# Kernel tuning notes

Measured on AMD Instinct MI355X. Metric: run time of the kernel, lower is better.

## Reference

```python
import jax, jax.numpy as jnp
import numpy as np

WIN = (9, 9)
EPS = float(np.power(np.e, -15))  # e^-15 threshold from original code


def _box_sum(x, win):
    kernel = jnp.ones((1, 1, win[0], win[1]), dtype=x.dtype)
    p = win[0] // 2
    return jax.lax.conv_general_dilated(
        x, kernel, window_strides=(1, 1), padding=[(p, p), (p, p)],
        dimension_numbers=("NCHW", "OIHW", "NCHW"))


def setup_inputs() -> dict:
    key = jax.random.key(0)
    k1, k2 = jax.random.split(key)
    B, C, H, W = 32, 1, 512, 512
    I = jax.random.normal(k1, (B, C, H, W), dtype=jnp.float32)
    J = jax.random.normal(k2, (B, C, H, W), dtype=jnp.float32)
    return {"I": I, "J": J}


def reference(I, J):
    win = WIN
    win_size = win[0] * win[1]
    I_sum = _box_sum(I, win)
    J_sum = _box_sum(J, win)
    I2_sum = _box_sum(I * I, win)
    J2_sum = _box_sum(J * J, win)
    IJ_sum = _box_sum(I * J, win)

    u_I = I_sum / win_size
    u_J = J_sum / win_size
    cross = IJ_sum - u_J * I_sum - u_I * J_sum + u_I * u_J * win_size
    I_var = I2_sum - 2 * u_I * I_sum + u_I * u_I * win_size
    J_var = J2_sum - 2 * u_J * J_sum + u_J * u_J * win_size

    non_zero = I_var * J_var > EPS
    cross = jnp.where(non_zero, cross, 1.0)
    I_var = jnp.where(non_zero, I_var, 1.0)
    J_var = jnp.where(non_zero, J_var, 1.0)

    cc = cross * cross / (I_var * J_var + EPS)
    return -1.0 * jnp.mean(cc, axis=(1, 2, 3)) + 1.0
```

## Files before the change

kernel.cpp:

```cpp
#include <hip/hip_runtime.h>


#define IMG_H 512
#define IMG_W 512
#define NBATCH 32
#define RPW 8
#define STRIPS_PER_IMG (IMG_H / RPW)

__global__ __launch_bounds__(64, 2) void lcc_main(const float* __restrict__ I,
                                                  const float* __restrict__ J,
                                                  float* __restrict__ out) {
    const int lane  = threadIdx.x;
    const int strip = blockIdx.x;
    const int b  = strip / STRIPS_PER_IMG;
    const int y0 = (strip % STRIPS_PER_IMG) * RPW;
    const int x0 = lane * 8;

    const float* __restrict__ Ib = I + (size_t)b * IMG_H * IMG_W;
    const float* __restrict__ Jb = J + (size_t)b * IMG_H * IMG_W;

    auto load_row = [&](int y, float4& i0, float4& i1, float4& j0, float4& j1) {
        const float4* pI = reinterpret_cast<const float4*>(Ib + (size_t)y * IMG_W + x0);
        const float4* pJ = reinterpret_cast<const float4*>(Jb + (size_t)y * IMG_W + x0);
        i0 = pI[0]; i1 = pI[1]; j0 = pJ[0]; j1 = pJ[1];
    };

    float sI[8]  = {0.f,0.f,0.f,0.f,0.f,0.f,0.f,0.f};
    float sJ[8]  = {0.f,0.f,0.f,0.f,0.f,0.f,0.f,0.f};
    float sII[8] = {0.f,0.f,0.f,0.f,0.f,0.f,0.f,0.f};
    float sJJ[8] = {0.f,0.f,0.f,0.f,0.f,0.f,0.f,0.f};
    float sIJ[8] = {0.f,0.f,0.f,0.f,0.f,0.f,0.f,0.f};

    auto addv = [&](const float4& i0, const float4& i1,
                    const float4& j0, const float4& j1) {
        float iv[8] = {i0.x,i0.y,i0.z,i0.w,i1.x,i1.y,i1.z,i1.w};
        float jv[8] = {j0.x,j0.y,j0.z,j0.w,j1.x,j1.y,j1.z,j1.w};
        #pragma unroll
        for (int c = 0; c < 8; ++c) {
            sI[c]  += iv[c];
            sJ[c]  += jv[c];
            sII[c]  = fmaf(iv[c], iv[c], sII[c]);
            sJJ[c]  = fmaf(jv[c], jv[c], sJJ[c]);
            sIJ[c]  = fmaf(iv[c], jv[c], sIJ[c]);
        }
    };
    auto subv = [&](const float4& i0, const float4& i1,
                    const float4& j0, const float4& j1) {
        float iv[8] = {i0.x,i0.y,i0.z,i0.w,i1.x,i1.y,i1.z,i1.w};
        float jv[8] = {j0.x,j0.y,j0.z,j0.w,j1.x,j1.y,j1.z,j1.w};
        #pragma unroll
        for (int c = 0; c < 8; ++c) {
            sI[c]  -= iv[c];
            sJ[c]  -= jv[c];
            sII[c]  = fmaf(-iv[c], iv[c], sII[c]);
            sJJ[c]  = fmaf(-jv[c], jv[c], sJJ[c]);
            sIJ[c]  = fmaf(-iv[c], jv[c], sIJ[c]);
        }
    };

    auto hsum = [&](const float (&s)[8], float (&h)[8]) {
        float w[16];
        #pragma unroll
        for (int c = 0; c < 8; ++c) w[4+c] = s[c];
        #pragma unroll
        for (int c = 0; c < 4; ++c) {
            float a = __shfl_up(s[4+c], 1);
            w[c] = lane ? a : 0.f;
            a = __shfl_down(s[c], 1);
            w[12+c] = (lane < 63) ? a : 0.f;
        }
        float acc = 0.f;
        #pragma unroll
        for (int i = 0; i < 9; ++i) acc += w[i];
        h[0] = acc;
        #pragma unroll
        for (int k = 1; k < 8; ++k) { acc += w[k+8] - w[k-1]; h[k] = acc; }
    };

    #pragma unroll
    for (int k = 0; k < 9; ++k) {
        const int y = y0 - 4 + k;
        if (y >= 0) {
            float4 i0, i1, j0, j1;
            load_row(y, i0, i1, j0, j1);
            addv(i0, i1, j0, j1);
        }
    }

    const float inv81 = 1.0f / 81.0f;
    const float EPSV  = 3.0590232050182579e-07f;
    float local = 0.0f;

    #pragma unroll 1
    for (int r = 0; r < RPW; ++r) {
        const int t = y0 + r;

        const bool doadd = (r + 1 < RPW) && (t + 5 < IMG_H);
        const bool dosub = (r + 1 < RPW) && (t - 4 >= 0);
        float4 ai0 = {0,0,0,0}, ai1 = {0,0,0,0}, aj0 = {0,0,0,0}, aj1 = {0,0,0,0};
        float4 bi0 = {0,0,0,0}, bi1 = {0,0,0,0}, bj0 = {0,0,0,0}, bj1 = {0,0,0,0};
        if (doadd) load_row(t + 5, ai0, ai1, aj0, aj1);
        if (dosub) load_row(t - 4, bi0, bi1, bj0, bj1);

        float hI[8], hJ[8], hII[8], hJJ[8], hIJ[8];
        hsum(sI,  hI);
        hsum(sJ,  hJ);
        hsum(sII, hII);
        hsum(sJJ, hJJ);
        hsum(sIJ, hIJ);

        #pragma unroll
        for (int k = 0; k < 8; ++k) {
            float cross = fmaf(hI[k] * hJ[k], -inv81, hIJ[k]);
            float Iv    = fmaf(hI[k] * hI[k], -inv81, hII[k]);
            float Jv    = fmaf(hJ[k] * hJ[k], -inv81, hJJ[k]);
            float p  = Iv * Jv;
            bool  nz = p > EPSV;
            float c2 = nz ? cross : 1.0f;
            float p2 = nz ? p : 1.0f;
            local += (c2 * c2) * __builtin_amdgcn_rcpf(p2 + EPSV);
        }

        if (doadd) addv(ai0, ai1, aj0, aj1);
        if (dosub) subv(bi0, bi1, bj0, bj1);
    }

    #pragma unroll
    for (int off = 32; off > 0; off >>= 1) local += __shfl_down(local, off);
    if (lane == 0)
        atomicAdd(out + b, fmaf(local, -1.0f / (float)(IMG_H * IMG_W),
                                1.0f / (float)STRIPS_PER_IMG));
}

extern "C" void kernel_launch(void* const* d_in, const int* in_sizes, int n_in,
                              void* d_out, int out_size, void* d_ws, size_t ws_size,
                              hipStream_t stream) {
    const float* I = (const float*)d_in[0];
    const float* J = (const float*)d_in[1];
    float* out = (float*)d_out;

    const int total_strips = NBATCH * STRIPS_PER_IMG;
    lcc_main<<<total_strips, 64, 0, stream>>>(I, J, out);
}
```

Baseline: 118.2 us.

## Cache window rows in registers and prefetch next add row ahead

The 9 initial window rows are held in a register array, so the rows later subtracted from the running sums come from registers instead of being loaded from global memory again. The row to be added is prefetched one iteration ahead, and the row loop is fully unrolled so those loads overlap with the box-sum compute. This targets memory latency and redundant traffic in a kernel with little occupancy to hide latency. The cost is much higher VGPR use, which could limit occupancy or cause spills.

```diff
diff --git a/kernel.cpp b/kernel.cpp
--- a/kernel.cpp
+++ b/kernel.cpp
@@ -19,10 +19,10 @@
     const float* __restrict__ Ib = I + (size_t)b * IMG_H * IMG_W;
     const float* __restrict__ Jb = J + (size_t)b * IMG_H * IMG_W;
 
-    auto load_row = [&](int y, float4& i0, float4& i1, float4& j0, float4& j1) {
+    auto load_row = [&](int y, float4* d) {
         const float4* pI = reinterpret_cast<const float4*>(Ib + (size_t)y * IMG_W + x0);
         const float4* pJ = reinterpret_cast<const float4*>(Jb + (size_t)y * IMG_W + x0);
-        i0 = pI[0]; i1 = pI[1]; j0 = pJ[0]; j1 = pJ[1];
+        d[0] = pI[0]; d[1] = pI[1]; d[2] = pJ[0]; d[3] = pJ[1];
     };
 
     float sI[8]  = {0.f,0.f,0.f,0.f,0.f,0.f,0.f,0.f};
@@ -31,10 +31,9 @@
     float sJJ[8] = {0.f,0.f,0.f,0.f,0.f,0.f,0.f,0.f};
     float sIJ[8] = {0.f,0.f,0.f,0.f,0.f,0.f,0.f,0.f};
 
-    auto addv = [&](const float4& i0, const float4& i1,
-                    const float4& j0, const float4& j1) {
-        float iv[8] = {i0.x,i0.y,i0.z,i0.w,i1.x,i1.y,i1.z,i1.w};
-        float jv[8] = {j0.x,j0.y,j0.z,j0.w,j1.x,j1.y,j1.z,j1.w};
+    auto addv = [&](const float4* v) {
+        float iv[8] = {v[0].x,v[0].y,v[0].z,v[0].w,v[1].x,v[1].y,v[1].z,v[1].w};
+        float jv[8] = {v[2].x,v[2].y,v[2].z,v[2].w,v[3].x,v[3].y,v[3].z,v[3].w};
         #pragma unroll
         for (int c = 0; c < 8; ++c) {
             sI[c]  += iv[c];
@@ -44,10 +43,9 @@
             sIJ[c]  = fmaf(iv[c], jv[c], sIJ[c]);
         }
     };
-    auto subv = [&](const float4& i0, const float4& i1,
-                    const float4& j0, const float4& j1) {
-        float iv[8] = {i0.x,i0.y,i0.z,i0.w,i1.x,i1.y,i1.z,i1.w};
-        float jv[8] = {j0.x,j0.y,j0.z,j0.w,j1.x,j1.y,j1.z,j1.w};
+    auto subv = [&](const float4* v) {
+        float iv[8] = {v[0].x,v[0].y,v[0].z,v[0].w,v[1].x,v[1].y,v[1].z,v[1].w};
+        float jv[8] = {v[2].x,v[2].y,v[2].z,v[2].w,v[3].x,v[3].y,v[3].z,v[3].w};
         #pragma unroll
         for (int c = 0; c < 8; ++c) {
             sI[c]  -= iv[c];
@@ -77,30 +75,34 @@
         for (int k = 1; k < 8; ++k) { acc += w[k+8] - w[k-1]; h[k] = acc; }
     };
 
+    float4 W[9][4];
     #pragma unroll
     for (int k = 0; k < 9; ++k) {
-        const int y = y0 - 4 + k;
-        if (y >= 0) {
-            float4 i0, i1, j0, j1;
-            load_row(y, i0, i1, j0, j1);
-            addv(i0, i1, j0, j1);
-        }
+        #pragma unroll
+        for (int q = 0; q < 4; ++q) W[k][q] = make_float4(0.f, 0.f, 0.f, 0.f);
     }
+    #pragma unroll
+    for (int k = 0; k < 9; ++k)
+        if (y0 - 4 + k >= 0) load_row(y0 - 4 + k, W[k]);
+
+    float4 acur[4];
+    load_row(y0 + 5, acur);
+    float4 anxt[4] = {{0,0,0,0},{0,0,0,0},{0,0,0,0},{0,0,0,0}};
+
+    #pragma unroll
+    for (int k = 0; k < 9; ++k)
+        if (y0 - 4 + k >= 0) addv(W[k]);
 
     const float inv81 = 1.0f / 81.0f;
     const float EPSV  = 3.0590232050182579e-07f;
     float local = 0.0f;
 
-    #pragma unroll 1
+    #pragma unroll
     for (int r = 0; r < RPW; ++r) {
         const int t = y0 + r;
 
-        const bool doadd = (r + 1 < RPW) && (t + 5 < IMG_H);
-        const bool dosub = (r + 1 < RPW) && (t - 4 >= 0);
-        float4 ai0 = {0,0,0,0}, ai1 = {0,0,0,0}, aj0 = {0,0,0,0}, aj1 = {0,0,0,0};
-        float4 bi0 = {0,0,0,0}, bi1 = {0,0,0,0}, bj0 = {0,0,0,0}, bj1 = {0,0,0,0};
-        if (doadd) load_row(t + 5, ai0, ai1, aj0, aj1);
-        if (dosub) load_row(t - 4, bi0, bi1, bj0, bj1);
+        const bool pfn = (r + 2 < RPW) && (t + 6 < IMG_H);
+        if (pfn) load_row(t + 6, anxt);
 
         float hI[8], hJ[8], hII[8], hJJ[8], hIJ[8];
         hsum(sI,  hI);
@@ -121,8 +123,14 @@
             local += (c2 * c2) * __builtin_amdgcn_rcpf(p2 + EPSV);
         }
 
-        if (doadd) addv(ai0, ai1, aj0, aj1);
-        if (dosub) subv(bi0, bi1, bj0, bj1);
+        if (r + 1 < RPW) {
+            if (t + 5 < IMG_H) addv(acur);
+            if (t - 4 >= 0)    subv(W[r]);
+            if (pfn) {
+                acur[0] = anxt[0]; acur[1] = anxt[1];
+                acur[2] = anxt[2]; acur[3] = anxt[3];
+            }
+        }
     }
 
     #pragma unroll
```

After: 240.0 us. 2.03x slower.

## Stage rows in LDS ring via global_load_lds and split images into column halves

Applied to the files above, without the earlier changes.

Each block now covers a 16-row by 256-column tile, with 4 output columns per lane. Rows are staged into a 9-slot LDS ring with async global_load_lds. Rows leaving the window are read back from LDS rather than reloaded from global memory, and the horizontal halo comes from overlapping loads, which replaces the cross-lane shuffles. The aim is to halve redundant global traffic for subtracted rows and to remove the shuffle-based horizontal sums. In exchange it adds halo loads at the tile edges, manual waitcnt synchronisation and LDS usage, and the hand-written waitcnt encodings risk ordering mistakes.

```diff
diff --git a/kernel.cpp b/kernel.cpp
--- a/kernel.cpp
+++ b/kernel.cpp
@@ -4,39 +4,101 @@
 #define IMG_H 512
 #define IMG_W 512
 #define NBATCH 32
-#define RPW 8
-#define STRIPS_PER_IMG (IMG_H / RPW)
+#define RPW 16
+#define STRIPS_Y (IMG_H / RPW)
+#define BLOCKS_PER_IMG (STRIPS_Y * 2)
+#define RING 9
+#define SLOT 512
+
+typedef __attribute__((address_space(3))) void       lds_t;
+typedef __attribute__((address_space(1))) const void glob_t;
 
 __global__ __launch_bounds__(64, 2) void lcc_main(const float* __restrict__ I,
                                                   const float* __restrict__ J,
                                                   float* __restrict__ out) {
-    const int lane  = threadIdx.x;
-    const int strip = blockIdx.x;
-    const int b  = strip / STRIPS_PER_IMG;
-    const int y0 = (strip % STRIPS_PER_IMG) * RPW;
-    const int x0 = lane * 8;
+    __shared__ __align__(16) float ring[RING][SLOT];
+
+    const int lane = threadIdx.x;
+    const int blk  = blockIdx.x;
+    const int b    = blk >> 6;
+    const int rem  = blk & 63;
+    const int y0   = (rem >> 1) * RPW;
+    const int c0   = (rem & 1) << 8;
+    const bool leftb = (c0 == 0);
+    const int hcol = leftb ? 256 : 252;
 
     const float* __restrict__ Ib = I + (size_t)b * IMG_H * IMG_W;
     const float* __restrict__ Jb = J + (size_t)b * IMG_H * IMG_W;
 
-    auto load_row = [&](int y, float4& i0, float4& i1, float4& j0, float4& j1) {
-        const float4* pI = reinterpret_cast<const float4*>(Ib + (size_t)y * IMG_W + x0);
-        const float4* pJ = reinterpret_cast<const float4*>(Jb + (size_t)y * IMG_W + x0);
-        i0 = pI[0]; i1 = pI[1]; j0 = pJ[0]; j1 = pJ[1];
-    };
-
-    float sI[8]  = {0.f,0.f,0.f,0.f,0.f,0.f,0.f,0.f};
-    float sJ[8]  = {0.f,0.f,0.f,0.f,0.f,0.f,0.f,0.f};
-    float sII[8] = {0.f,0.f,0.f,0.f,0.f,0.f,0.f,0.f};
-    float sJJ[8] = {0.f,0.f,0.f,0.f,0.f,0.f,0.f,0.f};
-    float sIJ[8] = {0.f,0.f,0.f,0.f,0.f,0.f,0.f,0.f};
-
-    auto addv = [&](const float4& i0, const float4& i1,
-                    const float4& j0, const float4& j1) {
-        float iv[8] = {i0.x,i0.y,i0.z,i0.w,i1.x,i1.y,i1.z,i1.w};
-        float jv[8] = {j0.x,j0.y,j0.z,j0.w,j1.x,j1.y,j1.z,j1.w};
-        #pragma unroll
-        for (int c = 0; c < 8; ++c) {
+    auto stage_row = [&](int y) {
+        int slot = (y - y0 + 4) % RING;
+        const float* gI = Ib + (size_t)y * IMG_W + c0;
+        const float* gJ = Jb + (size_t)y * IMG_W + c0;
+        __builtin_amdgcn_global_load_lds((glob_t*)(gI + lane * 4), (lds_t*)&ring[slot][0],   16, 0, 0);
+        __builtin_amdgcn_global_load_lds((glob_t*)(gJ + lane * 4), (lds_t*)&ring[slot][256], 16, 0, 0);
+    };
+
+    auto load_halo = [&](int y, float4& hi, float4& hj) {
+        hi = *reinterpret_cast<const float4*>(Ib + (size_t)y * IMG_W + hcol);
+        hj = *reinterpret_cast<const float4*>(Jb + (size_t)y * IMG_W + hcol);
+    };
+
+    float sI[12], sJ[12], sII[12], sJJ[12], sIJ[12];
+    #pragma unroll
+    for (int c = 0; c < 12; ++c) { sI[c]=0.f; sJ[c]=0.f; sII[c]=0.f; sJJ[c]=0.f; sIJ[c]=0.f; }
+
+    auto read_win = [&](int y, const float4 hi, const float4 hj,
+                        float (&iv)[12], float (&jv)[12]) {
+        int slot = (y - y0 + 4) % RING;
+        const float* base = &ring[slot][0];
+        const int kB = lane * 4;
+        const int kA = (lane == 0)  ? 0   : kB - 4;
+        const int kC = (lane == 63) ? 248 : kB + 4;
+        float4 iA = *reinterpret_cast<const float4*>(base + kA);
+        float4 iB = *reinterpret_cast<const float4*>(base + kB);
+        float4 iC = *reinterpret_cast<const float4*>(base + kC);
+        float4 jA = *reinterpret_cast<const float4*>(base + 256 + kA);
+        float4 jB = *reinterpret_cast<const float4*>(base + 256 + kB);
+        float4 jC = *reinterpret_cast<const float4*>(base + 256 + kC);
+        const bool lo0  = (lane == 0);
+        const bool hi63 = (lane == 63);
+        iv[0]=lo0?(leftb?0.f:hi.x):iA.x; iv[1]=lo0?(leftb?0.f:hi.y):iA.y;
+        iv[2]=lo0?(leftb?0.f:hi.z):iA.z; iv[3]=lo0?(leftb?0.f:hi.w):iA.w;
+        iv[4]=iB.x; iv[5]=iB.y; iv[6]=iB.z; iv[7]=iB.w;
+        iv[8]=hi63?(leftb?hi.x:0.f):iC.x; iv[9]=hi63?(leftb?hi.y:0.f):iC.y;
+        iv[10]=hi63?(leftb?hi.z:0.f):iC.z; iv[11]=hi63?(leftb?hi.w:0.f):iC.w;
+        jv[0]=lo0?(leftb?0.f:hj.x):jA.x; jv[1]=lo0?(leftb?0.f:hj.y):jA.y;
+        jv[2]=lo0?(leftb?0.f:hj.z):jA.z; jv[3]=lo0?(leftb?0.f:hj.w):jA.w;
+        jv[4]=jB.x; jv[5]=jB.y; jv[6]=jB.z; jv[7]=jB.w;
+        jv[8]=hi63?(leftb?hj.x:0.f):jC.x; jv[9]=hi63?(leftb?hj.y:0.f):jC.y;
+        jv[10]=hi63?(leftb?hj.z:0.f):jC.z; jv[11]=hi63?(leftb?hj.w:0.f):jC.w;
+    };
+
+    const bool killlo = leftb && (lane == 0);
+    const bool killhi = (!leftb) && (lane == 63);
+    auto load_row_reg = [&](int y, float (&iv)[12], float (&jv)[12]) {
+        const int cs = c0 + lane * 4 - 4;
+        const int r0 = killlo ? 0   : cs;
+        const int r2 = killhi ? 508 : cs + 8;
+        const float* rI = Ib + (size_t)y * IMG_W;
+        const float* rJ = Jb + (size_t)y * IMG_W;
+        float4 a  = *reinterpret_cast<const float4*>(rI + r0);
+        float4 b4 = *reinterpret_cast<const float4*>(rI + cs + 4);
+        float4 c4 = *reinterpret_cast<const float4*>(rI + r2);
+        float4 d  = *reinterpret_cast<const float4*>(rJ + r0);
+        float4 e4 = *reinterpret_cast<const float4*>(rJ + cs + 4);
+        float4 f4 = *reinterpret_cast<const float4*>(rJ + r2);
+        iv[0]=killlo?0.f:a.x; iv[1]=killlo?0.f:a.y; iv[2]=killlo?0.f:a.z; iv[3]=killlo?0.f:a.w;
+        iv[4]=b4.x; iv[5]=b4.y; iv[6]=b4.z; iv[7]=b4.w;
+        iv[8]=killhi?0.f:c4.x; iv[9]=killhi?0.f:c4.y; iv[10]=killhi?0.f:c4.z; iv[11]=killhi?0.f:c4.w;
+        jv[0]=killlo?0.f:d.x; jv[1]=killlo?0.f:d.y; jv[2]=killlo?0.f:d.z; jv[3]=killlo?0.f:d.w;
+        jv[4]=e4.x; jv[5]=e4.y; jv[6]=e4.z; jv[7]=e4.w;
+        jv[8]=killhi?0.f:f4.x; jv[9]=killhi?0.f:f4.y; jv[10]=killhi?0.f:f4.z; jv[11]=killhi?0.f:f4.w;
+    };
+
+    auto add12 = [&](const float (&iv)[12], const float (&jv)[12]) {
+        #pragma unroll
+        for (int c = 0; c < 12; ++c) {
             sI[c]  += iv[c];
             sJ[c]  += jv[c];
             sII[c]  = fmaf(iv[c], iv[c], sII[c]);
@@ -44,12 +106,9 @@
             sIJ[c]  = fmaf(iv[c], jv[c], sIJ[c]);
         }
     };
-    auto subv = [&](const float4& i0, const float4& i1,
-                    const float4& j0, const float4& j1) {
-        float iv[8] = {i0.x,i0.y,i0.z,i0.w,i1.x,i1.y,i1.z,i1.w};
-        float jv[8] = {j0.x,j0.y,j0.z,j0.w,j1.x,j1.y,j1.z,j1.w};
-        #pragma unroll
-        for (int c = 0; c < 8; ++c) {
+    auto sub12 = [&](const float (&iv)[12], const float (&jv)[12]) {
+        #pragma unroll
+        for (int c = 0; c < 12; ++c) {
             sI[c]  -= iv[c];
             sJ[c]  -= jv[c];
             sII[c]  = fmaf(-iv[c], iv[c], sII[c]);
@@ -58,32 +117,29 @@
         }
     };
 
-    auto hsum = [&](const float (&s)[8], float (&h)[8]) {
-        float w[16];
-        #pragma unroll
-        for (int c = 0; c < 8; ++c) w[4+c] = s[c];
-        #pragma unroll
-        for (int c = 0; c < 4; ++c) {
-            float a = __shfl_up(s[4+c], 1);
-            w[c] = lane ? a : 0.f;
-            a = __shfl_down(s[c], 1);
-            w[12+c] = (lane < 63) ? a : 0.f;
-        }
+    auto hsum = [&](const float (&s)[12], float (&h)[4]) {
         float acc = 0.f;
         #pragma unroll
-        for (int i = 0; i < 9; ++i) acc += w[i];
+        for (int i = 0; i < 9; ++i) acc += s[i];
         h[0] = acc;
         #pragma unroll
-        for (int k = 1; k < 8; ++k) { acc += w[k+8] - w[k-1]; h[k] = acc; }
-    };
-
+        for (int k = 1; k < 4; ++k) { acc += s[k+8] - s[k-1]; h[k] = acc; }
+    };
+
+    const int wy_lo = (y0 - 4 < 0) ? 0 : y0 - 4;
+    const int wy_hi = y0 + 4;
+    #pragma unroll 1
+    for (int y = wy_lo; y <= wy_hi; ++y) stage_row(y);
+    __builtin_amdgcn_s_waitcnt(0x3F70);
     #pragma unroll
     for (int k = 0; k < 9; ++k) {
         const int y = y0 - 4 + k;
         if (y >= 0) {
-            float4 i0, i1, j0, j1;
-            load_row(y, i0, i1, j0, j1);
-            addv(i0, i1, j0, j1);
+            float4 hi, hj;
+            load_halo(y, hi, hj);
+            float iv[12], jv[12];
+            read_win(y, hi, hj, iv, jv);
+            add12(iv, jv);
         }
     }
 
@@ -94,15 +150,15 @@
     #pragma unroll 1
     for (int r = 0; r < RPW; ++r) {
         const int t = y0 + r;
-
         const bool doadd = (r + 1 < RPW) && (t + 5 < IMG_H);
         const bool dosub = (r + 1 < RPW) && (t - 4 >= 0);
-        float4 ai0 = {0,0,0,0}, ai1 = {0,0,0,0}, aj0 = {0,0,0,0}, aj1 = {0,0,0,0};
-        float4 bi0 = {0,0,0,0}, bi1 = {0,0,0,0}, bj0 = {0,0,0,0}, bj1 = {0,0,0,0};
-        if (doadd) load_row(t + 5, ai0, ai1, aj0, aj1);
-        if (dosub) load_row(t - 4, bi0, bi1, bj0, bj1);
-
-        float hI[8], hJ[8], hII[8], hJJ[8], hIJ[8];
+
+        float aiv[12], ajv[12];
+        if (doadd) load_row_reg(t + 5, aiv, ajv);
+        float4 shi = {0,0,0,0}, shj = {0,0,0,0};
+        if (dosub) load_halo(t - 4, shi, shj);
+
+        float hI[4], hJ[4], hII[4], hJJ[4], hIJ[4];
         hsum(sI,  hI);
         hsum(sJ,  hJ);
         hsum(sII, hII);
@@ -110,7 +166,7 @@
         hsum(sIJ, hIJ);
 
         #pragma unroll
-        for (int k = 0; k < 8; ++k) {
+        for (int k = 0; k < 4; ++k) {
             float cross = fmaf(hI[k] * hJ[k], -inv81, hIJ[k]);
             float Iv    = fmaf(hI[k] * hI[k], -inv81, hII[k]);
             float Jv    = fmaf(hJ[k] * hJ[k], -inv81, hJJ[k]);
@@ -121,15 +177,23 @@
             local += (c2 * c2) * __builtin_amdgcn_rcpf(p2 + EPSV);
         }
 
-        if (doadd) addv(ai0, ai1, aj0, aj1);
-        if (dosub) subv(bi0, bi1, bj0, bj1);
+        if (dosub) {
+            float iv[12], jv[12];
+            read_win(t - 4, shi, shj, iv, jv);
+            sub12(iv, jv);
+        }
+        if (doadd) {
+            __builtin_amdgcn_s_waitcnt(0xC07F);
+            stage_row(t + 5);
+            add12(aiv, ajv);
+        }
     }
 
     #pragma unroll
     for (int off = 32; off > 0; off >>= 1) local += __shfl_down(local, off);
     if (lane == 0)
         atomicAdd(out + b, fmaf(local, -1.0f / (float)(IMG_H * IMG_W),
-                                1.0f / (float)STRIPS_PER_IMG));
+                                1.0f / (float)BLOCKS_PER_IMG));
 }
 
 extern "C" void kernel_launch(void* const* d_in, const int* in_sizes, int n_in,
@@ -139,6 +203,6 @@
     const float* J = (const float*)d_in[1];
     float* out = (float*)d_out;
 
-    const int total_strips = NBATCH * STRIPS_PER_IMG;
-    lcc_main<<<total_strips, 64, 0, stream>>>(I, J, out);
+    const int total_blocks = NBATCH * BLOCKS_PER_IMG;
+    lcc_main<<<total_blocks, 64, 0, stream>>>(I, J, out);
 }
```

Result: slower. 130.8 us (+10.7%).
